# Optimization experiments

Measured on AMD Instinct MI355X. Metric: run time of the kernel, lower is better.

Reference implementation:

```python
import jax, jax.numpy as jnp
import numpy as np

B, T, EMB = 2, 2048, 1024
H, D = 16, 64          # num_heads, head_dim; hidden = H*D = 1024
SCALE = D ** (-0.5)


def setup_inputs() -> dict:
    key = jax.random.key(0)
    k1, k2, k3, k4, k5 = jax.random.split(key, 5)
    return {
        "x":    jax.random.normal(k1, (B, T, EMB), dtype=jnp.float32),
        "Wqkv": jax.random.normal(k2, (EMB, 3 * H * D), dtype=jnp.float32) * (EMB ** -0.5),
        "bqkv": jax.random.normal(k3, (3 * H * D,), dtype=jnp.float32) * 0.02,
        "Wout": jax.random.normal(k4, (H * D, EMB), dtype=jnp.float32) * ((H * D) ** -0.5),
        "bout": jax.random.normal(k5, (EMB,), dtype=jnp.float32) * 0.02,
    }


def reference(x, Wqkv, bqkv, Wout, bout):
    b, t, _ = x.shape
    qkv = x @ Wqkv + bqkv                                   # [b, t, 3*H*D]
    q, k, v = jnp.split(qkv, 3, axis=-1)
    split_heads = lambda a: a.reshape(b, t, H, D).transpose(0, 2, 1, 3)  # [b,h,t,d]
    q, k, v = split_heads(q), split_heads(k), split_heads(v)

    scores = jnp.einsum('bhid,bhjd->bhij', q, k) * SCALE    # [b,h,t,t]
    causal = jnp.tril(jnp.ones((t, t), dtype=bool))         # lower-triangular mask
    scores = jnp.where(causal, scores, -jnp.inf)
    attn = jax.nn.softmax(scores, axis=-1)                  # dropout: eval mode (identity)

    out = jnp.einsum('bhij,bhjd->bhid', attn, v)            # [b,h,t,d]
    out = out.transpose(0, 2, 1, 3).reshape(b, t, H * D)    # [b,t,H*D]
    return out @ Wout + bout                                # [b,t,EMB]
```

## Files before the change

### kernel.cpp

```cpp
#include <hip/hip_runtime.h>
#include <hip/hip_bf16.h>
#include <stdint.h>

#define B_ 2
#define T_ 2048
#define EMB_ 1024
#define H_ 16
#define D_ 64
#define QS_ 0.1803368801111f

typedef __attribute__((ext_vector_type(8))) __bf16 bf8_t;
typedef __attribute__((ext_vector_type(8))) short s8_t;
typedef __attribute__((ext_vector_type(4))) short s4_t;
typedef __attribute__((ext_vector_type(4))) float f4_t;
typedef __attribute__((ext_vector_type(2))) unsigned int u32x2;

#if __has_builtin(__builtin_amdgcn_exp2f)
#define EXP2(x) __builtin_amdgcn_exp2f(x)
#else
#define EXP2(x) exp2f(x)
#endif

__device__ __forceinline__ short f2b(float f) {
    union { float f; uint32_t u; } c; c.f = f;
    uint32_t r = (c.u + 0x7FFFu + ((c.u >> 16) & 1u)) >> 16;
    return (short)(uint16_t)r;
}

__device__ __forceinline__ uint32_t cvtpk(float lo, float hi) {
    uint32_t r;
    asm volatile("v_cvt_pk_bf16_f32 %0, %1, %2" : "=v"(r) : "v"(lo), "v"(hi));
    return r;
}

__device__ __forceinline__ void glds16(const void* g, void* l) {
    __builtin_amdgcn_global_load_lds(
        (const __attribute__((address_space(1))) unsigned int*)g,
        (__attribute__((address_space(3))) unsigned int*)l, 16, 0, 0);
}

__global__ __launch_bounds__(256)
void cast_f32_bf16(const float* __restrict__ in, short* __restrict__ outp) {
    const size_t i = ((size_t)blockIdx.x * 256 + threadIdx.x) * 4;
    f4_t v = *(const f4_t*)(in + i);
    s4_t r; r[0] = f2b(v[0]); r[1] = f2b(v[1]); r[2] = f2b(v[2]); r[3] = f2b(v[3]);
    *(s4_t*)(outp + i) = r;
}

__global__ __launch_bounds__(256)
void transpose_f2b(const float* __restrict__ in, short* __restrict__ outp,
                   int K, int N, int nscale, float sc) {
    __shared__ short Ts[64][72];
    const int t = threadIdx.x;
    const int r = t >> 4, c = (t & 15) * 4;
    const int n0 = blockIdx.x * 64, k0 = blockIdx.y * 64;
    #pragma unroll
    for (int it = 0; it < 4; it++) {
        const int rr = it * 16 + r;
        f4_t v = *(const f4_t*)(in + (size_t)(k0 + rr) * N + n0 + c);
        #pragma unroll
        for (int j = 0; j < 4; j++) {
            const float s = (n0 + c + j < nscale) ? sc : 1.0f;
            Ts[c + j][rr] = f2b(v[j] * s);
        }
    }
    __syncthreads();
    #pragma unroll
    for (int it = 0; it < 4; it++) {
        const int rr = it * 16 + r;
        s4_t o;
        #pragma unroll
        for (int j = 0; j < 4; j++) o[j] = Ts[rr][c + j];
        *(s4_t*)(outp + (size_t)(n0 + rr) * K + k0 + c) = o;
    }
}

__global__ __launch_bounds__(256)
void transpose_v(const short* __restrict__ qkv, short* __restrict__ vt) {
    __shared__ short Ts[64][72];
    const int t = threadIdx.x;
    const int r = t >> 4, c = (t & 15) * 4;
    const int bh = blockIdx.y, bb = bh >> 4, hh = bh & 15;
    const int t0 = blockIdx.x * 64;
    #pragma unroll
    for (int it = 0; it < 4; it++) {
        const int rr = it * 16 + r;
        s4_t v = *(const s4_t*)(qkv + (size_t)(bb * T_ + t0 + rr) * 3072 + 2048 + hh * 64 + c);
        #pragma unroll
        for (int j = 0; j < 4; j++) Ts[c + j][rr] = v[j];
    }
    __syncthreads();
    #pragma unroll
    for (int it = 0; it < 4; it++) {
        const int rr = it * 16 + r;
        s4_t o;
        #pragma unroll
        for (int j = 0; j < 4; j++) o[j] = Ts[rr][c + j];
        *(s4_t*)(vt + (size_t)(bh * 64 + rr) * T_ + t0 + c) = o;
    }
}

__global__ __launch_bounds__(256)
void gemm_bt(const short* __restrict__ A, const short* __restrict__ Bt,
             const float* __restrict__ bias, short* __restrict__ Cb,
             float* __restrict__ Cf, int M, int N, int K, int outf32, int qsflag)
{
    __shared__ __align__(16) short As[128 * 64];
    __shared__ __align__(16) short Bs[128 * 64];

    const int t = threadIdx.x;
    const int L = t & 63, l16 = L & 15, quad = L >> 4;
    const int w = t >> 6, wm = w >> 1, wn = w & 1;
    const int n0 = blockIdx.x * 128, m0 = blockIdx.y * 128;

    f4_t acc[4][4];
    #pragma unroll
    for (int i = 0; i < 4; i++)
        #pragma unroll
        for (int j = 0; j < 4; j++) acc[i][j] = (f4_t){0.f, 0.f, 0.f, 0.f};

    for (int k0 = 0; k0 < K; k0 += 64) {
        __syncthreads();
        #pragma unroll
        for (int it = 0; it < 4; it++) {
            const int c = it * 256 + t;
            const int row = c >> 3, pc = c & 7;
            const int cc = pc ^ (row & 7);
            glds16(A + (size_t)(m0 + row) * K + k0 + cc * 8, &As[c * 8]);
            glds16(Bt + (size_t)(n0 + row) * K + k0 + cc * 8, &Bs[c * 8]);
        }
        asm volatile("s_waitcnt vmcnt(0)" ::: "memory");
        __syncthreads();

        #pragma unroll
        for (int kc = 0; kc < 2; kc++) {
            bf8_t a[4], b[4];
            #pragma unroll
            for (int i = 0; i < 4; i++) {
                const int row = wm * 64 + i * 16 + l16;
                const int ch = (kc * 4 + quad) ^ (row & 7);
                a[i] = *(const bf8_t*)(&As[row * 64 + ch * 8]);
            }
            #pragma unroll
            for (int j = 0; j < 4; j++) {
                const int row = wn * 64 + j * 16 + l16;
                const int ch = (kc * 4 + quad) ^ (row & 7);
                b[j] = *(const bf8_t*)(&Bs[row * 64 + ch * 8]);
            }
            #pragma unroll
            for (int i = 0; i < 4; i++)
                #pragma unroll
                for (int j = 0; j < 4; j++)
                    acc[i][j] = __builtin_amdgcn_mfma_f32_16x16x32_bf16(a[i], b[j], acc[i][j], 0, 0, 0);
        }
    }

    #pragma unroll
    for (int j = 0; j < 4; j++) {
        const int n = n0 + wn * 64 + j * 16 + l16;
        float bv = bias[n];
        if (qsflag && n < 1024) bv *= QS_;
        #pragma unroll
        for (int i = 0; i < 4; i++) {
            #pragma unroll
            for (int r = 0; r < 4; r++) {
                const int m = m0 + wm * 64 + i * 16 + quad * 4 + r;
                const float val = acc[i][j][r] + bv;
                if (outf32) Cf[(size_t)m * N + n] = val;
                else        Cb[(size_t)m * N + n] = f2b(val);
            }
        }
    }
}

__global__ __launch_bounds__(256)
void attn_kernel(const short* __restrict__ qkv, const short* __restrict__ vt,
                 short* __restrict__ ab)
{
    __shared__ __align__(16) short Ks[2][64 * 64];
    __shared__ __align__(16) short Vs[2][64 * 64];
    __shared__ __align__(16) short Ps[4][16 * 64];

    const int t = threadIdx.x;
    const int L = t & 63, l16 = L & 15, quad = L >> 4;
    const int w = t >> 6;

    const int qi = 31 - (blockIdx.x >> 5);
    const int bh = blockIdx.x & 31;
    const int bb = bh >> 4, hh = bh & 15;
    const int qb = qi * 64;
    const int wrow = qb + w * 16;
    const int qrow = wrow + l16;

    const size_t qoff = (size_t)(bb * T_ + wrow + l16) * 3072 + hh * 64;
    const bf8_t qa0 = *(const bf8_t*)(qkv + qoff + quad * 8);
    const bf8_t qa1 = *(const bf8_t*)(qkv + qoff + 32 + quad * 8);

    s8_t os_;
    #pragma unroll
    for (int i = 0; i < 8; i++) os_[i] = (short)0x3F80;
    const bf8_t ones = *(const bf8_t*)&os_;

    f4_t lacc = {0.f, 0.f, 0.f, 0.f};
    f4_t o_acc[4];
    #pragma unroll
    for (int nc = 0; nc < 4; nc++) o_acc[nc] = (f4_t){0.f, 0.f, 0.f, 0.f};

#define STAGE(ktile, buf)                                                      \
    {                                                                          \
        const int ktb_ = (ktile) * 64;                                         \
        _Pragma("unroll")                                                      \
        for (int it = 0; it < 2; it++) {                                       \
            const int c = it * 256 + t;                                        \
            const int row = c >> 3, pc = c & 7;                                \
            const int cc = pc ^ (row & 7);                                     \
            glds16(qkv + (size_t)(bb * T_ + ktb_ + row) * 3072 + 1024 + hh * 64 + cc * 8, \
                   &Ks[buf][c * 8]);                                           \
            glds16(vt + (size_t)(bh * 64 + row) * T_ + ktb_ + cc * 8,          \
                   &Vs[buf][c * 8]);                                           \
        }                                                                      \
    }

    const int nkt = qi + 1;
    STAGE(0, 0);
    for (int kt = 0; kt < nkt; kt++) {
        const int cur = kt & 1;
        if (kt + 1 < nkt) {
            STAGE(kt + 1, cur ^ 1);
            asm volatile("s_waitcnt vmcnt(4)" ::: "memory");
        } else {
            asm volatile("s_waitcnt vmcnt(0)" ::: "memory");
        }
        __builtin_amdgcn_s_barrier();

        if (kt * 64 <= wrow + 15) {
            const int ktb = kt * 64;
            const bool domask = (ktb + 63 > wrow);

            f4_t s[4];
            #pragma unroll
            for (int nh = 0; nh < 4; nh++) {
                const int key = nh * 16 + l16;
                const int ch0 = quad ^ (key & 7);
                const int ch1 = (4 + quad) ^ (key & 7);
                bf8_t k0f = *(const bf8_t*)(&Ks[cur][key * 64 + ch0 * 8]);
                bf8_t k1f = *(const bf8_t*)(&Ks[cur][key * 64 + ch1 * 8]);
                f4_t z = {0.f, 0.f, 0.f, 0.f};
                z = __builtin_amdgcn_mfma_f32_16x16x32_bf16(k0f, qa0, z, 0, 0, 0);
                z = __builtin_amdgcn_mfma_f32_16x16x32_bf16(k1f, qa1, z, 0, 0, 0);
                s[nh] = z;
            }

            char* const psb = (char*)&Ps[w][0];
            #pragma unroll
            for (int nh = 0; nh < 4; nh++) {
                float v0 = s[nh][0], v1 = s[nh][1], v2 = s[nh][2], v3 = s[nh][3];
                if (domask) {
                    const int keyb = ktb + nh * 16 + quad * 4;
                    if (keyb     > qrow) v0 = -1e30f;
                    if (keyb + 1 > qrow) v1 = -1e30f;
                    if (keyb + 2 > qrow) v2 = -1e30f;
                    if (keyb + 3 > qrow) v3 = -1e30f;
                }
                u32x2 pk2;
                pk2.x = cvtpk(EXP2(v0), EXP2(v1));
                pk2.y = cvtpk(EXP2(v2), EXP2(v3));
                *(u32x2*)(psb + l16 * 128 + ((nh * 32 + quad * 8) ^ ((l16 & 7) << 4))) = pk2;
            }
            asm volatile("s_waitcnt lgkmcnt(0)" ::: "memory");

            const bf8_t pa0 = *(const bf8_t*)(psb + l16 * 128 + ((quad * 16) ^ ((l16 & 7) << 4)));
            const bf8_t pa1 = *(const bf8_t*)(psb + l16 * 128 + ((64 + quad * 16) ^ ((l16 & 7) << 4)));

            lacc = __builtin_amdgcn_mfma_f32_16x16x32_bf16(pa0, ones, lacc, 0, 0, 0);
            lacc = __builtin_amdgcn_mfma_f32_16x16x32_bf16(pa1, ones, lacc, 0, 0, 0);

            #pragma unroll
            for (int nc = 0; nc < 4; nc++) {
                const int d = nc * 16 + l16;
                const int ch0 = quad ^ (d & 7);
                const int ch1 = (4 + quad) ^ (d & 7);
                bf8_t v0f = *(const bf8_t*)(&Vs[cur][d * 64 + ch0 * 8]);
                bf8_t v1f = *(const bf8_t*)(&Vs[cur][d * 64 + ch1 * 8]);
                o_acc[nc] = __builtin_amdgcn_mfma_f32_16x16x32_bf16(pa0, v0f, o_acc[nc], 0, 0, 0);
                o_acc[nc] = __builtin_amdgcn_mfma_f32_16x16x32_bf16(pa1, v1f, o_acc[nc], 0, 0, 0);
            }
        }
        __builtin_amdgcn_s_barrier();
    }
#undef STAGE

    #pragma unroll
    for (int r = 0; r < 4; r++) {
        const float rl = __builtin_amdgcn_rcpf(lacc[r]);
        const int row = wrow + quad * 4 + r;
        #pragma unroll
        for (int nc = 0; nc < 4; nc++) {
            ab[(size_t)(bb * T_ + row) * 1024 + hh * 64 + nc * 16 + l16] =
                f2b(o_acc[nc][r] * rl);
        }
    }
}

extern "C" void kernel_launch(void* const* d_in, const int* in_sizes, int n_in,
                              void* d_out, int out_size, void* d_ws, size_t ws_size,
                              hipStream_t stream) {
    const float* x    = (const float*)d_in[0];
    const float* Wqkv = (const float*)d_in[1];
    const float* bqkv = (const float*)d_in[2];
    const float* Wout = (const float*)d_in[3];
    const float* bout = (const float*)d_in[4];
    float* out = (float*)d_out;

    short* ws   = (short*)d_ws;
    short* xb   = ws;
    short* wqt  = xb + (size_t)4096 * 1024;
    short* qkvt = wqt + (size_t)3072 * 1024;
    short* vt   = (short*)d_out;
    short* ab   = xb;

    cast_f32_bf16<<<4096, 256, 0, stream>>>(x, xb);
    transpose_f2b<<<dim3(48, 16), 256, 0, stream>>>(Wqkv, wqt, 1024, 3072, 1024, QS_);

    gemm_bt<<<dim3(24, 32), 256, 0, stream>>>(xb, wqt, bqkv, qkvt, nullptr,
                                              4096, 3072, 1024, 0, 1);

    transpose_v<<<dim3(32, 32), 256, 0, stream>>>(qkvt, vt);
    transpose_f2b<<<dim3(16, 16), 256, 0, stream>>>(Wout, wqt, 1024, 1024, 0, 1.0f);

    attn_kernel<<<1024, 256, 0, stream>>>(qkvt, vt, ab);

    gemm_bt<<<dim3(8, 32), 256, 0, stream>>>(ab, wqt, bout, nullptr, out,
                                             4096, 1024, 1024, 1, 0);
}
```

Baseline: 189.8 us.

## Process 128 query rows per attention block with two 16-row tiles per wave

The attention kernel now handles 128 query rows per block, each wave owning two 16-row query tiles, so every K/V tile staged into shared memory is reused across twice as many queries. K and V fragments are loaded into registers once per tile and applied to both query subtiles, which halves global K/V traffic and LDS reads per unit of work. The grid halves to 512 blocks, and register pressure (two sets of accumulators plus cached K/V fragments) and per-block imbalance along the causal diagonal both increase.

```diff
diff --git a/kernel.cpp b/kernel.cpp
--- a/kernel.cpp
+++ b/kernel.cpp
@@ -179,32 +179,37 @@
 {
     __shared__ __align__(16) short Ks[2][64 * 64];
     __shared__ __align__(16) short Vs[2][64 * 64];
-    __shared__ __align__(16) short Ps[4][16 * 64];
+    __shared__ __align__(16) short Ps[4][2 * 1024];
 
     const int t = threadIdx.x;
     const int L = t & 63, l16 = L & 15, quad = L >> 4;
     const int w = t >> 6;
 
-    const int qi = 31 - (blockIdx.x >> 5);
+    const int qi = 15 - (blockIdx.x >> 5);
     const int bh = blockIdx.x & 31;
     const int bb = bh >> 4, hh = bh & 15;
-    const int qb = qi * 64;
-    const int wrow = qb + w * 16;
-    const int qrow = wrow + l16;
-
-    const size_t qoff = (size_t)(bb * T_ + wrow + l16) * 3072 + hh * 64;
-    const bf8_t qa0 = *(const bf8_t*)(qkv + qoff + quad * 8);
-    const bf8_t qa1 = *(const bf8_t*)(qkv + qoff + 32 + quad * 8);
+    const int qb = qi * 128;
+    const int wrow = qb + w * 32;
+
+    const size_t qoff0 = (size_t)(bb * T_ + wrow + l16) * 3072 + hh * 64;
+    const size_t qoff1 = qoff0 + (size_t)16 * 3072;
+    const bf8_t q0a = *(const bf8_t*)(qkv + qoff0 + quad * 8);
+    const bf8_t q0b = *(const bf8_t*)(qkv + qoff0 + 32 + quad * 8);
+    const bf8_t q1a = *(const bf8_t*)(qkv + qoff1 + quad * 8);
+    const bf8_t q1b = *(const bf8_t*)(qkv + qoff1 + 32 + quad * 8);
 
     s8_t os_;
     #pragma unroll
     for (int i = 0; i < 8; i++) os_[i] = (short)0x3F80;
     const bf8_t ones = *(const bf8_t*)&os_;
 
-    f4_t lacc = {0.f, 0.f, 0.f, 0.f};
-    f4_t o_acc[4];
-    #pragma unroll
-    for (int nc = 0; nc < 4; nc++) o_acc[nc] = (f4_t){0.f, 0.f, 0.f, 0.f};
+    f4_t lacc0 = {0.f, 0.f, 0.f, 0.f}, lacc1 = {0.f, 0.f, 0.f, 0.f};
+    f4_t o_acc0[4], o_acc1[4];
+    #pragma unroll
+    for (int nc = 0; nc < 4; nc++) {
+        o_acc0[nc] = (f4_t){0.f, 0.f, 0.f, 0.f};
+        o_acc1[nc] = (f4_t){0.f, 0.f, 0.f, 0.f};
+    }
 
 #define STAGE(ktile, buf)                                                      \
     {                                                                          \
@@ -221,7 +226,7 @@
         }                                                                      \
     }
 
-    const int nkt = qi + 1;
+    const int nkt = 2 * qi + 2;
     STAGE(0, 0);
     for (int kt = 0; kt < nkt; kt++) {
         const int cur = kt & 1;
@@ -233,57 +238,101 @@
         }
         __builtin_amdgcn_s_barrier();
 
-        if (kt * 64 <= wrow + 15) {
-            const int ktb = kt * 64;
-            const bool domask = (ktb + 63 > wrow);
-
-            f4_t s[4];
+        const int ktb = kt * 64;
+        if (ktb <= wrow + 31) {
+            const bool do0 = (ktb <= wrow + 15);
+            char* const psb = (char*)&Ps[w][0];
+            const int swz = (l16 & 7) << 4;
+
+            bf8_t k0f[4], k1f[4];
             #pragma unroll
             for (int nh = 0; nh < 4; nh++) {
                 const int key = nh * 16 + l16;
                 const int ch0 = quad ^ (key & 7);
                 const int ch1 = (4 + quad) ^ (key & 7);
-                bf8_t k0f = *(const bf8_t*)(&Ks[cur][key * 64 + ch0 * 8]);
-                bf8_t k1f = *(const bf8_t*)(&Ks[cur][key * 64 + ch1 * 8]);
-                f4_t z = {0.f, 0.f, 0.f, 0.f};
-                z = __builtin_amdgcn_mfma_f32_16x16x32_bf16(k0f, qa0, z, 0, 0, 0);
-                z = __builtin_amdgcn_mfma_f32_16x16x32_bf16(k1f, qa1, z, 0, 0, 0);
-                s[nh] = z;
-            }
-
-            char* const psb = (char*)&Ps[w][0];
-            #pragma unroll
-            for (int nh = 0; nh < 4; nh++) {
-                float v0 = s[nh][0], v1 = s[nh][1], v2 = s[nh][2], v3 = s[nh][3];
-                if (domask) {
-                    const int keyb = ktb + nh * 16 + quad * 4;
-                    if (keyb     > qrow) v0 = -1e30f;
-                    if (keyb + 1 > qrow) v1 = -1e30f;
-                    if (keyb + 2 > qrow) v2 = -1e30f;
-                    if (keyb + 3 > qrow) v3 = -1e30f;
+                k0f[nh] = *(const bf8_t*)(&Ks[cur][key * 64 + ch0 * 8]);
+                k1f[nh] = *(const bf8_t*)(&Ks[cur][key * 64 + ch1 * 8]);
+            }
+
+            if (do0) {
+                const int qrow = wrow + l16;
+                const bool domask = (ktb + 63 > wrow);
+                #pragma unroll
+                for (int nh = 0; nh < 4; nh++) {
+                    f4_t z = {0.f, 0.f, 0.f, 0.f};
+                    z = __builtin_amdgcn_mfma_f32_16x16x32_bf16(k0f[nh], q0a, z, 0, 0, 0);
+                    z = __builtin_amdgcn_mfma_f32_16x16x32_bf16(k1f[nh], q0b, z, 0, 0, 0);
+                    float v0 = z[0], v1 = z[1], v2 = z[2], v3 = z[3];
+                    if (domask) {
+                        const int keyb = ktb + nh * 16 + quad * 4;
+                        if (keyb     > qrow) v0 = -1e30f;
+                        if (keyb + 1 > qrow) v1 = -1e30f;
+                        if (keyb + 2 > qrow) v2 = -1e30f;
+                        if (keyb + 3 > qrow) v3 = -1e30f;
+                    }
+                    u32x2 pk2;
+                    pk2.x = cvtpk(EXP2(v0), EXP2(v1));
+                    pk2.y = cvtpk(EXP2(v2), EXP2(v3));
+                    *(u32x2*)(psb + l16 * 128 + ((nh * 32 + quad * 8) ^ swz)) = pk2;
                 }
-                u32x2 pk2;
-                pk2.x = cvtpk(EXP2(v0), EXP2(v1));
-                pk2.y = cvtpk(EXP2(v2), EXP2(v3));
-                *(u32x2*)(psb + l16 * 128 + ((nh * 32 + quad * 8) ^ ((l16 & 7) << 4))) = pk2;
+            }
+
+            {
+                const int wrow1 = wrow + 16;
+                const int qrow = wrow1 + l16;
+                const bool domask = (ktb + 63 > wrow1);
+                #pragma unroll
+                for (int nh = 0; nh < 4; nh++) {
+                    f4_t z = {0.f, 0.f, 0.f, 0.f};
+                    z = __builtin_amdgcn_mfma_f32_16x16x32_bf16(k0f[nh], q1a, z, 0, 0, 0);
+                    z = __builtin_amdgcn_mfma_f32_16x16x32_bf16(k1f[nh], q1b, z, 0, 0, 0);
+                    float v0 = z[0], v1 = z[1], v2 = z[2], v3 = z[3];
+                    if (domask) {
+                        const int keyb = ktb + nh * 16 + quad * 4;
+                        if (keyb     > qrow) v0 = -1e30f;
+                        if (keyb + 1 > qrow) v1 = -1e30f;
+                        if (keyb + 2 > qrow) v2 = -1e30f;
+                        if (keyb + 3 > qrow) v3 = -1e30f;
+                    }
+                    u32x2 pk2;
+                    pk2.x = cvtpk(EXP2(v0), EXP2(v1));
+                    pk2.y = cvtpk(EXP2(v2), EXP2(v3));
+                    *(u32x2*)(psb + 2048 + l16 * 128 + ((nh * 32 + quad * 8) ^ swz)) = pk2;
+                }
             }
             asm volatile("s_waitcnt lgkmcnt(0)" ::: "memory");
 
-            const bf8_t pa0 = *(const bf8_t*)(psb + l16 * 128 + ((quad * 16) ^ ((l16 & 7) << 4)));
-            const bf8_t pa1 = *(const bf8_t*)(psb + l16 * 128 + ((64 + quad * 16) ^ ((l16 & 7) << 4)));
-
-            lacc = __builtin_amdgcn_mfma_f32_16x16x32_bf16(pa0, ones, lacc, 0, 0, 0);
-            lacc = __builtin_amdgcn_mfma_f32_16x16x32_bf16(pa1, ones, lacc, 0, 0, 0);
-
+            bf8_t v0f[4], v1f[4];
             #pragma unroll
             for (int nc = 0; nc < 4; nc++) {
                 const int d = nc * 16 + l16;
                 const int ch0 = quad ^ (d & 7);
                 const int ch1 = (4 + quad) ^ (d & 7);
-                bf8_t v0f = *(const bf8_t*)(&Vs[cur][d * 64 + ch0 * 8]);
-                bf8_t v1f = *(const bf8_t*)(&Vs[cur][d * 64 + ch1 * 8]);
-                o_acc[nc] = __builtin_amdgcn_mfma_f32_16x16x32_bf16(pa0, v0f, o_acc[nc], 0, 0, 0);
-                o_acc[nc] = __builtin_amdgcn_mfma_f32_16x16x32_bf16(pa1, v1f, o_acc[nc], 0, 0, 0);
+                v0f[nc] = *(const bf8_t*)(&Vs[cur][d * 64 + ch0 * 8]);
+                v1f[nc] = *(const bf8_t*)(&Vs[cur][d * 64 + ch1 * 8]);
+            }
+
+            if (do0) {
+                const bf8_t pa0 = *(const bf8_t*)(psb + l16 * 128 + ((quad * 16) ^ swz));
+                const bf8_t pa1 = *(const bf8_t*)(psb + l16 * 128 + ((64 + quad * 16) ^ swz));
+                lacc0 = __builtin_amdgcn_mfma_f32_16x16x32_bf16(pa0, ones, lacc0, 0, 0, 0);
+                lacc0 = __builtin_amdgcn_mfma_f32_16x16x32_bf16(pa1, ones, lacc0, 0, 0, 0);
+                #pragma unroll
+                for (int nc = 0; nc < 4; nc++) {
+                    o_acc0[nc] = __builtin_amdgcn_mfma_f32_16x16x32_bf16(pa0, v0f[nc], o_acc0[nc], 0, 0, 0);
+                    o_acc0[nc] = __builtin_amdgcn_mfma_f32_16x16x32_bf16(pa1, v1f[nc], o_acc0[nc], 0, 0, 0);
+                }
+            }
+            {
+                const bf8_t pa0 = *(const bf8_t*)(psb + 2048 + l16 * 128 + ((quad * 16) ^ swz));
+                const bf8_t pa1 = *(const bf8_t*)(psb + 2048 + l16 * 128 + ((64 + quad * 16) ^ swz));
+                lacc1 = __builtin_amdgcn_mfma_f32_16x16x32_bf16(pa0, ones, lacc1, 0, 0, 0);
+                lacc1 = __builtin_amdgcn_mfma_f32_16x16x32_bf16(pa1, ones, lacc1, 0, 0, 0);
+                #pragma unroll
+                for (int nc = 0; nc < 4; nc++) {
+                    o_acc1[nc] = __builtin_amdgcn_mfma_f32_16x16x32_bf16(pa0, v0f[nc], o_acc1[nc], 0, 0, 0);
+                    o_acc1[nc] = __builtin_amdgcn_mfma_f32_16x16x32_bf16(pa1, v1f[nc], o_acc1[nc], 0, 0, 0);
+                }
             }
         }
         __builtin_amdgcn_s_barrier();
@@ -292,12 +341,16 @@
 
     #pragma unroll
     for (int r = 0; r < 4; r++) {
-        const float rl = __builtin_amdgcn_rcpf(lacc[r]);
-        const int row = wrow + quad * 4 + r;
+        const float rl0 = __builtin_amdgcn_rcpf(lacc0[r]);
+        const float rl1 = __builtin_amdgcn_rcpf(lacc1[r]);
+        const int row0 = wrow + quad * 4 + r;
+        const int row1 = wrow + 16 + quad * 4 + r;
         #pragma unroll
         for (int nc = 0; nc < 4; nc++) {
-            ab[(size_t)(bb * T_ + row) * 1024 + hh * 64 + nc * 16 + l16] =
-                f2b(o_acc[nc][r] * rl);
+            ab[(size_t)(bb * T_ + row0) * 1024 + hh * 64 + nc * 16 + l16] =
+                f2b(o_acc0[nc][r] * rl0);
+            ab[(size_t)(bb * T_ + row1) * 1024 + hh * 64 + nc * 16 + l16] =
+                f2b(o_acc1[nc][r] * rl1);
         }
     }
 }
@@ -328,7 +381,7 @@
     transpose_v<<<dim3(32, 32), 256, 0, stream>>>(qkvt, vt);
     transpose_f2b<<<dim3(16, 16), 256, 0, stream>>>(Wout, wqt, 1024, 1024, 0, 1.0f);
 
-    attn_kernel<<<1024, 256, 0, stream>>>(qkvt, vt, ab);
+    attn_kernel<<<512, 256, 0, stream>>>(qkvt, vt, ab);
 
     gemm_bt<<<dim3(8, 32), 256, 0, stream>>>(ab, wqt, bout, nullptr, out,
                                              4096, 1024, 1024, 1, 0);
```

Result: slower. 204.0 us (+7.5%).
